# Performance work log

Measured on AMD Instinct MI355X. Metric: run time of the kernel, lower is better.

## Reference

```python
import jax, jax.numpy as jnp
import numpy as np

# static module hyperparameters (match init_kwargs)
DIMS = 1024
HEAD = 16
HD = DIMS // HEAD          # 64
MAX_ITER = 3
MIN_SIZE = 64
MAX_SIZE = 2048
UP_WIN, DOWN_WIN = 1.1, 0.9
UP_DIFF, DOWN_DIFF = 0.05, 0.001
B, T = 2, 1024


def _ln(x, w, eps=1e-5):
    # torch LayerNorm with bias=False (weight only), biased variance
    m = jnp.mean(x, axis=-1, keepdims=True)
    v = jnp.var(x, axis=-1, keepdims=True)
    return (x - m) * jax.lax.rsqrt(v + eps) * w


def setup_inputs() -> dict:
    key = jax.random.key(0)
    ks = jax.random.split(key, 12)

    def lin_w(k, o, i):
        return (jax.random.normal(k, (o, i), dtype=jnp.float32) / np.sqrt(i)).astype(jnp.float32)

    return {
        "x": jax.random.normal(ks[0], (B, T, DIMS), dtype=jnp.float32),
        "Wq": lin_w(ks[1], DIMS, DIMS), "bq": jnp.zeros((DIMS,), jnp.float32),
        "Wk": lin_w(ks[2], DIMS, DIMS),
        "Wv": lin_w(ks[3], DIMS, DIMS), "bv": jnp.zeros((DIMS,), jnp.float32),
        "Wo": lin_w(ks[4], DIMS, DIMS), "bo": jnp.zeros((DIMS,), jnp.float32),
        "lna_w": jnp.ones((DIMS,), jnp.float32),
        "lnb_w": jnp.ones((DIMS,), jnp.float32),
        "lnc_w": jnp.ones((HD,), jnp.float32),
        "lnd_w": jnp.ones((HD,), jnp.float32),
        "lq_w": lin_w(ks[5], HD, HD), "lq_b": jnp.zeros((HD,), jnp.float32),
        "lk_w": lin_w(ks[6], HD, HD), "lk_b": jnp.zeros((HD,), jnp.float32),
        "lv_w": lin_w(ks[7], HD, HD), "lv_b": jnp.zeros((HD,), jnp.float32),
        "threshold": jnp.float32(0.01),
        "temp_base": jnp.float32(1.0),
        "factor": jnp.float32(0.1),
    }


def _focus(x, Wq, bq, Wk, Wv, bv, Wo, bo, lna_w, lnb_w, lnc_w, lnd_w,
           lq_w, lq_b, lk_w, lk_b, lv_w, lv_b, threshold, temp_base, factor):
    b, t, d = x.shape
    q = _ln(x, lna_w) @ Wq.T + bq
    kk = _ln(x, lnb_w) @ Wk.T
    v = _ln(x, lnb_w) @ Wv.T + bv
    sc = HD ** (-0.25)

    def _shape(u):
        return u.reshape(b, t, HEAD, HD).transpose(0, 2, 1, 3)  # [B,H,T,hd]

    q_full = _shape(q * sc)
    k_full = _shape(kk * sc)
    v_full = _shape(v)

    # .item() calls in torch detach these from the graph
    thr = jax.lax.stop_gradient(threshold)
    fac = jax.lax.stop_gradient(factor)
    t0 = jax.lax.stop_gradient(temp_base)

    cw0 = jnp.int32(max(min(t, MAX_SIZE), MIN_SIZE))
    inv_sqrt_e = jnp.float32(1.0 / np.sqrt(HD))  # SDPA default scale
    pos = jnp.arange(t)

    def step(carry, i):
        qcur, prev, attn, cw, temp, done = carry
        # LocalOut projections over full length (out-of-window part masked below)
        qp = qcur @ lq_w.T + lq_b
        kp = k_full @ lk_w.T + lk_b
        vp = v_full @ lv_w.T + lv_b
        sq = _ln(qp, lnc_w)
        sk = _ln(kp, lnd_w)
        tscale = jnp.where(temp > 0, jax.lax.rsqrt(temp), jnp.float32(1.0))
        sq = sq * tscale
        scores = jnp.einsum('bhqd,bhkd->bhqk', sq, sk) * inv_sqrt_e
        in_win = pos < cw
        scores = jnp.where(in_win[None, None, None, :], scores, -jnp.inf)
        probs = jax.nn.softmax(scores, axis=-1)
        out = jnp.einsum('bhqk,bhkd->bhqd', probs, vp)
        # rows >= cur_win stay zero (iter_out buffer semantics)
        iter_out = jnp.where(in_win[None, None, :, None], out, 0.0)

        diff = jnp.mean(jnp.abs(iter_out - prev))
        converged = (diff < thr + fac * diff) & (i > 0)
        upd = (~done) & (~converged)            # continue iterating
        new_done = done | converged

        attn_n = jnp.where(done, attn, iter_out)
        prev_n = jnp.where(upd, iter_out, prev)
        qcur_n = jnp.where(upd, qcur + iter_out, qcur)
        # _next_win
        up = (cw.astype(jnp.float32) * UP_WIN).astype(jnp.int32)
        down = (cw.astype(jnp.float32) * DOWN_WIN).astype(jnp.int32)
        nw = jnp.where(diff > UP_DIFF, up,
                       jnp.where((diff < DOWN_DIFF) & (cw > MIN_SIZE), down, cw))
        nw = jnp.clip(nw, MIN_SIZE, t)
        cw_n = jnp.where(upd, nw, cw)
        temp_n = jnp.where(upd, temp + jnp.float32(0.005), temp)
        return (qcur_n, prev_n, attn_n, cw_n, temp_n, new_done), None

    zeros = jnp.zeros_like(q_full)
    carry0 = (q_full, zeros, zeros, cw0, t0, jnp.array(False))
    (_, _, attn_out, _, _, _), _ = jax.lax.scan(step, carry0, jnp.arange(MAX_ITER))

    output = attn_out.transpose(0, 2, 1, 3).reshape(b, t, d)
    return output @ Wo.T + bo


def reference(x, Wq, bq, Wk, Wv, bv, Wo, bo, lna_w, lnb_w, lnc_w, lnd_w,
              lq_w, lq_b, lk_w, lk_b, lv_w, lv_b, threshold, temp_base, factor):
    return _focus(x, Wq, bq, Wk, Wv, bv, Wo, bo, lna_w, lnb_w, lnc_w, lnd_w,
                  lq_w, lq_b, lk_w, lk_b, lv_w, lv_b, threshold, temp_base, factor)
```

## Files before the change

### kernel.cpp

```cpp
#include <hip/hip_runtime.h>
#include <hip/hip_bf16.h>

#define BDIM 2
#define TDIM 1024
#define DDIM 1024
#define HDIM 16
#define HD   64
#define RROWS (BDIM * TDIM)
#define BH    (BDIM * HDIM)
#define NHE   (BH * TDIM * HD)
#define NHE4  (NHE / 4)
#define DIFF_BLOCKS 512
#define L2E 1.4426950408889634f

typedef __attribute__((ext_vector_type(8))) short short8v;
typedef __attribute__((ext_vector_type(4))) short short4v;
typedef __attribute__((ext_vector_type(8))) _Float16 half8v;
typedef __attribute__((ext_vector_type(4))) _Float16 half4v;
typedef __attribute__((ext_vector_type(4))) float f32x4;

struct FState {
  int   cw;
  float temp;
  int   done;
  int   upd;
  int   done_prev;
  float thr;
  float fac;
  int   pad;
};

static __device__ __forceinline__ unsigned short f2bf(float x) {
  __hip_bfloat16 h = __float2bfloat16(x);
  return __builtin_bit_cast(unsigned short, h);
}
static __device__ __forceinline__ void gload16(const void* g, void* l) {
  __builtin_amdgcn_global_load_lds(
      (const __attribute__((address_space(1))) void*)g,
      (__attribute__((address_space(3))) void*)l, 16, 0, 0);
}

__global__ void init_kernel(FState* st, const float* thr, const float* tb, const float* fac) {
  if (threadIdx.x == 0 && blockIdx.x == 0) {
    st->cw = TDIM;
    st->temp = tb[0];
    st->done = 0;
    st->done_prev = 0;
    st->upd = 1;
    st->thr = thr[0];
    st->fac = fac[0];
  }
}

__global__ __launch_bounds__(256) void ln_x_kernel(
    const float* __restrict__ x, const float* __restrict__ wa, const float* __restrict__ wb,
    _Float16* __restrict__ xaH, _Float16* __restrict__ xbH)
{
  const int row = blockIdx.x;
  const int tid = threadIdx.x;
  const float4 v = reinterpret_cast<const float4*>(x + (size_t)row * DDIM)[tid];
  float s = v.x + v.y + v.z + v.w;
  float q = v.x * v.x + v.y * v.y + v.z * v.z + v.w * v.w;
#pragma unroll
  for (int off = 1; off < 64; off <<= 1) {
    s += __shfl_xor(s, off);
    q += __shfl_xor(q, off);
  }
  __shared__ float ss[4], qq[4];
  const int lane = tid & 63, wv = tid >> 6;
  if (lane == 0) { ss[wv] = s; qq[wv] = q; }
  __syncthreads();
  s = ss[0] + ss[1] + ss[2] + ss[3];
  q = qq[0] + qq[1] + qq[2] + qq[3];
  const float mean = s * (1.0f / DDIM);
  const float var  = q * (1.0f / DDIM) - mean * mean;
  const float inv  = rsqrtf(var + 1e-5f);
  const float4 a4 = reinterpret_cast<const float4*>(wa)[tid];
  const float4 b4 = reinterpret_cast<const float4*>(wb)[tid];
  const float hv[4] = { (v.x - mean) * inv, (v.y - mean) * inv,
                        (v.z - mean) * inv, (v.w - mean) * inv };
  const float av[4] = { a4.x, a4.y, a4.z, a4.w };
  const float bv[4] = { b4.x, b4.y, b4.z, b4.w };
  half4v ha, hb;
#pragma unroll
  for (int j = 0; j < 4; ++j) {
    ha[j] = (_Float16)(hv[j] * av[j]);
    hb[j] = (_Float16)(hv[j] * bv[j]);
  }
  *reinterpret_cast<half4v*>(xaH + (size_t)row * DDIM + tid * 4) = ha;
  *reinterpret_cast<half4v*>(xbH + (size_t)row * DDIM + tid * 4) = hb;
}

__global__ __launch_bounds__(256) void w_cvt_kernel(
    const float* __restrict__ W0, const float* __restrict__ W1,
    const float* __restrict__ W2, const float* __restrict__ W3,
    const float* __restrict__ W4,
    _Float16* __restrict__ O0, _Float16* __restrict__ O1,
    _Float16* __restrict__ O2, _Float16* __restrict__ O3,
    _Float16* __restrict__ O4)
{
  const float* W; _Float16* O;
  switch (blockIdx.y) {
    case 0:  W = W0; O = O0; break;
    case 1:  W = W1; O = O1; break;
    case 2:  W = W2; O = O2; break;
    case 3:  W = W3; O = O3; break;
    default:
      if (blockIdx.x >= 4) return;
      W = W4; O = O4; break;
  }
  const int r = blockIdx.x;
  const int tid = threadIdx.x;
  const float4 v = reinterpret_cast<const float4*>(W + (size_t)r * 1024)[tid];
  half4v h;
  h[0] = (_Float16)v.x; h[1] = (_Float16)v.y;
  h[2] = (_Float16)v.z; h[3] = (_Float16)v.w;
  *reinterpret_cast<half4v*>(O + (size_t)r * 1024 + tid * 4) = h;
}

template<int CMODE>
__global__ __launch_bounds__(256) void gemm_mfma_kernel(
    const _Float16* __restrict__ A0, const _Float16* __restrict__ W0,
    const float* __restrict__ b0, float* __restrict__ C0, float s0,
    const _Float16* __restrict__ A1, const _Float16* __restrict__ W1,
    const float* __restrict__ b1, float* __restrict__ C1, float s1,
    const _Float16* __restrict__ A2, const _Float16* __restrict__ W2,
    const float* __restrict__ b2, float* __restrict__ C2, float s2)
{
  const _Float16* A; const _Float16* W; const float* bias; float* C; float scale;
  switch (blockIdx.z) {
    case 0:  A = A0; W = W0; bias = b0; C = C0; scale = s0; break;
    case 1:  A = A1; W = W1; bias = b1; C = C1; scale = s1; break;
    default: A = A2; W = W2; bias = b2; C = C2; scale = s2; break;
  }
  __shared__ __align__(16) _Float16 As[128 * 32];
  __shared__ __align__(16) _Float16 Ws[128 * 32];
  const int tid = threadIdx.x;
  const int wv = tid >> 6, lane = tid & 63;
  const int wm = wv >> 1, wn = wv & 1;
  const int bm = blockIdx.x;
  const int bn = blockIdx.y;

  const _Float16* gA[2]; const _Float16* gW[2];
  _Float16* lA[2]; _Float16* lW[2];
#pragma unroll
  for (int j = 0; j < 2; ++j) {
    const int chunk = wv * 2 + j;
    const int r = chunk * 16 + (lane >> 2);
    const int ce = (lane & 3) * 8;
    gA[j] = A + (size_t)(bm * 128 + r) * 1024 + ce;
    gW[j] = W + (size_t)(bn * 128 + r) * 1024 + ce;
    lA[j] = As + chunk * 512;
    lW[j] = Ws + chunk * 512;
  }

  f32x4 acc[4][4] = {};
  const int rb = lane & 15;
  const int kb = (lane >> 4) * 8;

  for (int ks = 0; ks < 1024; ks += 32) {
    __syncthreads();
#pragma unroll
    for (int j = 0; j < 2; ++j) {
      gload16(gA[j] + ks, lA[j]);
      gload16(gW[j] + ks, lW[j]);
    }
    __syncthreads();
    half8v af[4], wf[4];
#pragma unroll
    for (int f = 0; f < 4; ++f) {
      af[f] = *reinterpret_cast<const half8v*>(As + (wm * 64 + f * 16 + rb) * 32 + kb);
      wf[f] = *reinterpret_cast<const half8v*>(Ws + (wn * 64 + f * 16 + rb) * 32 + kb);
    }
#pragma unroll
    for (int i = 0; i < 4; ++i)
#pragma unroll
      for (int j2 = 0; j2 < 4; ++j2)
        acc[i][j2] = __builtin_amdgcn_mfma_f32_16x16x32_f16(af[i], wf[j2], acc[i][j2], 0, 0, 0);
  }

#pragma unroll
  for (int j2 = 0; j2 < 4; ++j2) {
    const int n = bn * 128 + wn * 64 + j2 * 16 + (lane & 15);
    const float bv_ = bias ? bias[n] : 0.0f;
#pragma unroll
    for (int i = 0; i < 4; ++i) {
#pragma unroll
      for (int r = 0; r < 4; ++r) {
        const int m = bm * 128 + wm * 64 + i * 16 + (lane >> 4) * 4 + r;
        const float v = (acc[i][j2][r] + bv_) * scale;
        size_t ci;
        if constexpr (CMODE == 0) {
          ci = (size_t)m * 1024 + n;
        } else {
          const int b = m >> 10, t = m & (TDIM - 1);
          ci = ((size_t)(b * HDIM + (n >> 6)) * TDIM + t) * HD + (n & 63);
        }
        C[ci] = v;
      }
    }
  }
}

template<int OUT_MODE, bool DO_LN>
static __device__ __forceinline__ void headproj_body(
    const float* __restrict__ in, unsigned short* __restrict__ out,
    const float* __restrict__ w, const float* __restrict__ bias,
    const float* __restrict__ lnw, float* wl, unsigned short* tT)
{
  const int tid = threadIdx.x;
  for (int idx = tid; idx < 4096; idx += 256) {
    const int d = idx >> 6, i = idx & 63;
    wl[i * 65 + d] = w[idx];
  }
  const int lane = tid & 63, wv = tid >> 6;
  const float bd = bias[lane];
  float lw = 1.0f;
  if constexpr (DO_LN) lw = lnw[lane];
  __syncthreads();
  const int rowBase = blockIdx.x * 32 + wv * 8;
  for (int rr = 0; rr < 8; ++rr) {
    const int row = rowBase + rr;
    const float h = in[(size_t)row * HD + lane];
    float y = bd;
#pragma unroll
    for (int i = 0; i < 64; ++i) {
      const float hv = __uint_as_float((unsigned)__builtin_amdgcn_readlane((int)__float_as_uint(h), i));
      y += wl[i * 65 + lane] * hv;
    }
    if constexpr (DO_LN) {
      float s = y;
#pragma unroll
      for (int off = 1; off < 64; off <<= 1) s += __shfl_xor(s, off);
      const float mean = s * (1.0f / 64.0f);
      const float t0 = y - mean;
      float v2 = t0 * t0;
#pragma unroll
      for (int off = 1; off < 64; off <<= 1) v2 += __shfl_xor(v2, off);
      y = t0 * rsqrtf(v2 * (1.0f / 64.0f) + 1e-5f) * lw;
    }
    if constexpr (OUT_MODE == 0) {
      out[(size_t)row * HD + lane] = f2bf(y);
    } else {
      tT[lane * 34 + wv * 8 + rr] = f2bf(y);
    }
  }
  if constexpr (OUT_MODE == 1) {
    __syncthreads();
    const int hd = tid >> 2, tseg = (tid & 3) * 8;
    const int r0 = blockIdx.x * 32;
    const int bh = r0 >> 10, t0 = r0 & (TDIM - 1);
    short8v v;
#pragma unroll
    for (int i = 0; i < 8; ++i) v[i] = (short)tT[hd * 34 + tseg + i];
    *reinterpret_cast<short8v*>(out + ((size_t)bh * HD + hd) * TDIM + t0 + tseg) = v;
  }
}

__global__ __launch_bounds__(256) void headproj_kv_kernel(
    const float* __restrict__ kin, unsigned short* __restrict__ skb,
    const float* __restrict__ lkw, const float* __restrict__ lkb,
    const float* __restrict__ lnd,
    const float* __restrict__ vin, unsigned short* __restrict__ vpT,
    const float* __restrict__ lvw, const float* __restrict__ lvb)
{
  __shared__ float wl[64 * 65];
  __shared__ unsigned short tT[64 * 34];
  if (blockIdx.y == 0)
    headproj_body<0, true >(kin, skb, lkw, lkb, lnd, wl, tT);
  else
    headproj_body<1, false>(vin, vpT, lvw, lvb, (const float*)nullptr, wl, tT);
}

__global__ __launch_bounds__(256) void attn_mfma_kernel(
    const float* __restrict__ qcur, const unsigned short* __restrict__ sk,
    const unsigned short* __restrict__ vpT, float* __restrict__ io,
    const float* __restrict__ prev, _Float16* __restrict__ attnH,
    const _Float16* __restrict__ lqwH, const float* __restrict__ lqb,
    const float* __restrict__ lnc, float* __restrict__ partials,
    const FState* __restrict__ st, int is_first)
{
  if (st->done) return;
  const int lid = blockIdx.x;
  const int xcd = lid & 7;
  const int rr_ = lid >> 3;
  const int qb  = rr_ & 15;
  const int bh  = (rr_ >> 4) * 8 + xcd;

  const int cw = st->cw;
  const int tid = threadIdx.x;
  const int wv = tid >> 6, lane = tid & 63;
  const int ql = lane & 15, hi = lane >> 4;
  const int qbase = qb * 64 + wv * 16;
  const int q = qbase + ql;
  const size_t baseRow = (size_t)bh * TDIM * HD;
  const size_t baseT   = (size_t)bh * HD * TDIM;
  float* orow = io + baseRow + (size_t)q * HD;
  const float* prow = prev + baseRow + (size_t)q * HD;
  float* qcrow = const_cast<float*>(qcur) + baseRow + (size_t)q * HD;
  const bool wvalid = (qbase < cw);
  _Float16* arow = attnH + (size_t)((bh >> 4) * TDIM + q) * 1024 + (bh & 15) * HD;

  __shared__ __align__(16) unsigned short Kt[2][64 * 64];
  __shared__ __align__(16) unsigned short Vt[2][64 * 64];
  __shared__ __align__(16) unsigned char Plds[4 * 2048];
  __shared__ float wred[4];

  const int sub  = lane >> 3;
  const int colB = (lane & 7) * 16;
  const int scol = (colB ^ (sub << 4)) >> 1;
  const unsigned short* kSrc0 = sk  + baseRow + (size_t)(wv * 16 + sub) * HD + scol;
  const unsigned short* vSrc0 = vpT + baseT  + (size_t)(wv * 16 + sub) * TDIM + scol;

  unsigned char* P = Plds + wv * 2048;
  const unsigned swz = (unsigned)((ql & 7) << 4);
  const unsigned rsw = swz;

#pragma unroll
  for (int jj = 0; jj < 2; ++jj) {
    const int j = wv * 2 + jj;
    gload16(kSrc0 + (size_t)(jj * 8) * HD, &Kt[0][j * 512]);
    gload16(vSrc0 + (size_t)(jj * 8) * TDIM + 0, &Vt[0][j * 512]);
  }

  short8v qf0, qf1;
  if (wvalid) {
    const float tp = st->temp;
    const float ts = (tp > 0.0f ? rsqrtf(tp) : 1.0f) * 0.125f;
    half8v qh0, qh1;
    {
      const f32x4 a0 = *reinterpret_cast<const f32x4*>(qcrow + hi * 8);
      const f32x4 a1 = *reinterpret_cast<const f32x4*>(qcrow + hi * 8 + 4);
      const f32x4 b0 = *reinterpret_cast<const f32x4*>(qcrow + 32 + hi * 8);
      const f32x4 b1 = *reinterpret_cast<const f32x4*>(qcrow + 32 + hi * 8 + 4);
#pragma unroll
      for (int j = 0; j < 4; ++j) {
        qh0[j] = (_Float16)a0[j]; qh0[4 + j] = (_Float16)a1[j];
        qh1[j] = (_Float16)b0[j]; qh1[4 + j] = (_Float16)b1[j];
      }
    }
    f32x4 sp[4];
#pragma unroll
    for (int f = 0; f < 4; ++f) {
      const half8v a0 = *reinterpret_cast<const half8v*>(lqwH + (f * 16 + ql) * 64 + hi * 8);
      const half8v a1 = *reinterpret_cast<const half8v*>(lqwH + (f * 16 + ql) * 64 + 32 + hi * 8);
      f32x4 acc = {};
      acc = __builtin_amdgcn_mfma_f32_16x16x32_f16(a0, qh0, acc, 0, 0, 0);
      acc = __builtin_amdgcn_mfma_f32_16x16x32_f16(a1, qh1, acc, 0, 0, 0);
      sp[f] = acc;
    }
    float sum = 0.f;
#pragma unroll
    for (int f = 0; f < 4; ++f) {
      const f32x4 b4 = *reinterpret_cast<const f32x4*>(lqb + f * 16 + hi * 4);
      sp[f] += b4;
      sum += (sp[f][0] + sp[f][1]) + (sp[f][2] + sp[f][3]);
    }
    sum += __shfl_xor(sum, 16);
    sum += __shfl_xor(sum, 32);
    const float mean = sum * (1.0f / 64.0f);
    float vs = 0.f;
#pragma unroll
    for (int f = 0; f < 4; ++f) {
#pragma unroll
      for (int r = 0; r < 4; ++r) {
        const float t0 = sp[f][r] - mean;
        sp[f][r] = t0;
        vs += t0 * t0;
      }
    }
    vs += __shfl_xor(vs, 16);
    vs += __shfl_xor(vs, 32);
    const float inv = rsqrtf(vs * (1.0f / 64.0f) + 1e-5f);
    const unsigned wb = (unsigned)(ql * 128 + hi * 8);
#pragma unroll
    for (int f = 0; f < 4; ++f) {
      const f32x4 lc = *reinterpret_cast<const f32x4*>(lnc + f * 16 + hi * 4);
      const float y0 = sp[f][0] * inv * lc[0] * ts;
      const float y1 = sp[f][1] * inv * lc[1] * ts;
      const float y2 = sp[f][2] * inv * lc[2] * ts;
      const float y3 = sp[f][3] * inv * lc[3] * ts;
      *reinterpret_cast<unsigned*>(P + ((wb + f * 32)     ^ swz)) =
          (unsigned)f2bf(y0) | ((unsigned)f2bf(y1) << 16);
      *reinterpret_cast<unsigned*>(P + ((wb + f * 32 + 4) ^ swz)) =
          (unsigned)f2bf(y2) | ((unsigned)f2bf(y3) << 16);
    }
    qf0 = *reinterpret_cast<short8v*>(P + ((unsigned)(ql * 128 + hi * 16) ^ swz));
    qf1 = *reinterpret_cast<short8v*>(P + ((unsigned)(ql * 128 + 64 + hi * 16) ^ swz));
  }
  __syncthreads();

  float m = -1e30f, l = 0.f;
  f32x4 o[4] = {};
  const int nch = (cw + 63) >> 6;
  int cur = 0;
  for (int ch = 0; ch < nch; ++ch) {
    const int k0 = ch * 64;
    if (ch + 1 < nch) {
      const int kn = (ch + 1) * 64;
#pragma unroll
      for (int jj = 0; jj < 2; ++jj) {
        const int j = wv * 2 + jj;
        gload16(kSrc0 + (size_t)(kn + jj * 8) * HD, &Kt[cur ^ 1][j * 512]);
        gload16(vSrc0 + (size_t)(jj * 8) * TDIM + kn, &Vt[cur ^ 1][j * 512]);
      }
    }
    if (wvalid) {
      const unsigned char* kt = (const unsigned char*)&Kt[cur][0];
      const unsigned char* vt = (const unsigned char*)&Vt[cur][0];
      f32x4 s[4];
#pragma unroll
      for (int f = 0; f < 4; ++f) {
        const unsigned rb = (unsigned)((f * 16 + ql) * 128);
        const short8v a0 = *reinterpret_cast<const short8v*>(kt + rb + ((unsigned)(hi * 16) ^ rsw));
        const short8v a1 = *reinterpret_cast<const short8v*>(kt + rb + ((unsigned)(64 + hi * 16) ^ rsw));
        f32x4 acc = {};
        acc = __builtin_amdgcn_mfma_f32_16x16x32_bf16(a0, qf0, acc, 0, 0, 0);
        acc = __builtin_amdgcn_mfma_f32_16x16x32_bf16(a1, qf1, acc, 0, 0, 0);
        s[f] = acc;
      }
      float mc = -1e30f;
#pragma unroll
      for (int f = 0; f < 4; ++f) {
#pragma unroll
        for (int r = 0; r < 4; ++r) {
          float v = s[f][r];
          if (k0 + f * 16 + hi * 4 + r >= cw) v = -1e30f;
          s[f][r] = v;
          mc = fmaxf(mc, v);
        }
      }
      mc = fmaxf(mc, __shfl_xor(mc, 16));
      mc = fmaxf(mc, __shfl_xor(mc, 32));
      const float mn = fmaxf(m, mc);
      const float c = __builtin_amdgcn_exp2f((m - mn) * L2E);
      float ls = 0.f;
      unsigned pk[8];
#pragma unroll
      for (int f = 0; f < 4; ++f) {
        const float p0 = __builtin_amdgcn_exp2f((s[f][0] - mn) * L2E);
        const float p1 = __builtin_amdgcn_exp2f((s[f][1] - mn) * L2E);
        const float p2 = __builtin_amdgcn_exp2f((s[f][2] - mn) * L2E);
        const float p3 = __builtin_amdgcn_exp2f((s[f][3] - mn) * L2E);
        ls += (p0 + p1) + (p2 + p3);
        pk[f * 2]     = (unsigned)f2bf(p0) | ((unsigned)f2bf(p1) << 16);
        pk[f * 2 + 1] = (unsigned)f2bf(p2) | ((unsigned)f2bf(p3) << 16);
      }
      ls += __shfl_xor(ls, 16);
      ls += __shfl_xor(ls, 32);
      l = l * c + ls;
      m = mn;
#pragma unroll
      for (int f = 0; f < 4; ++f) o[f] *= c;
      const unsigned wb = (unsigned)(ql * 128 + hi * 8);
#pragma unroll
      for (int f = 0; f < 4; ++f) {
        *reinterpret_cast<unsigned*>(P + ((wb + f * 32)     ^ swz)) = pk[f * 2];
        *reinterpret_cast<unsigned*>(P + ((wb + f * 32 + 4) ^ swz)) = pk[f * 2 + 1];
      }
#pragma unroll
      for (int kh = 0; kh < 2; ++kh) {
        const short8v pb = *reinterpret_cast<short8v*>(
            P + ((unsigned)(ql * 128 + kh * 64 + hi * 16) ^ swz));
#pragma unroll
        for (int f = 0; f < 4; ++f) {
          const unsigned rb = (unsigned)((f * 16 + ql) * 128);
          const short8v av = *reinterpret_cast<const short8v*>(
              vt + rb + ((unsigned)(kh * 64 + hi * 16) ^ rsw));
          o[f] = __builtin_amdgcn_mfma_f32_16x16x32_bf16(av, pb, o[f], 0, 0, 0);
        }
      }
    }
    __syncthreads();
    cur ^= 1;
  }

  float pd = 0.0f;
  if (wvalid) {
    const bool valid = (q < cw);
    const float invl = valid ? (1.0f / l) : 0.0f;
#pragma unroll
    for (int f = 0; f < 4; ++f) {
      const f32x4 vo = o[f] * invl;
      *reinterpret_cast<f32x4*>(orow + f * 16 + hi * 4) = vo;
      half4v h4;
      h4[0] = (_Float16)vo[0]; h4[1] = (_Float16)vo[1];
      h4[2] = (_Float16)vo[2]; h4[3] = (_Float16)vo[3];
      *reinterpret_cast<half4v*>(arow + f * 16 + hi * 4) = h4;
      const f32x4 qv = *reinterpret_cast<const f32x4*>(qcrow + f * 16 + hi * 4);
      *reinterpret_cast<f32x4*>(qcrow + f * 16 + hi * 4) = qv + vo;
      if (!is_first) {
        const f32x4 pv = *reinterpret_cast<const f32x4*>(prow + f * 16 + hi * 4);
        pd += fabsf(vo[0] - pv[0]) + fabsf(vo[1] - pv[1]) +
              fabsf(vo[2] - pv[2]) + fabsf(vo[3] - pv[3]);
      } else {
        pd += fabsf(vo[0]) + fabsf(vo[1]) + fabsf(vo[2]) + fabsf(vo[3]);
      }
    }
  } else {
    const f32x4 z = {0.f, 0.f, 0.f, 0.f};
    const half4v hz = { (_Float16)0.f, (_Float16)0.f, (_Float16)0.f, (_Float16)0.f };
#pragma unroll
    for (int f = 0; f < 4; ++f) {
      *reinterpret_cast<f32x4*>(orow + f * 16 + hi * 4) = z;
      *reinterpret_cast<half4v*>(arow + f * 16 + hi * 4) = hz;
      if (!is_first) {
        const f32x4 pv = *reinterpret_cast<const f32x4*>(prow + f * 16 + hi * 4);
        pd += fabsf(pv[0]) + fabsf(pv[1]) + fabsf(pv[2]) + fabsf(pv[3]);
      }
    }
  }

#pragma unroll
  for (int off = 1; off < 64; off <<= 1) pd += __shfl_xor(pd, off);
  if (lane == 0) wred[wv] = pd;
  __syncthreads();
  if (tid == 0)
    partials[lid] = wred[0] + wred[1] + wred[2] + wred[3];
}

__global__ __launch_bounds__(256) void state_update_kernel(
    FState* __restrict__ st, const float* __restrict__ partials, int iter)
{
  const int tid = threadIdx.x;
  float s = 0.0f;
  for (int i = tid; i < DIFF_BLOCKS; i += 256) s += partials[i];
  __shared__ float red[256];
  red[tid] = s;
  __syncthreads();
  for (int off = 128; off > 0; off >>= 1) {
    if (tid < off) red[tid] += red[tid + off];
    __syncthreads();
  }
  if (tid == 0) {
    const int done_prev = st->done;
    st->done_prev = done_prev;
    if (!done_prev) {
      const float diff = red[0] * (1.0f / (float)NHE);
      const bool conv = (diff < st->thr + st->fac * diff) && (iter > 0);
      st->upd  = conv ? 0 : 1;
      st->done = conv ? 1 : 0;
      if (!conv) {
        const int cw = st->cw;
        const int up = (int)((float)cw * 1.1f);
        const int dn = (int)((float)cw * 0.9f);
        int nw = (diff > 0.05f) ? up : ((diff < 0.001f && cw > 64) ? dn : cw);
        nw = nw < 64 ? 64 : (nw > TDIM ? TDIM : nw);
        st->cw = nw;
        st->temp += 0.005f;
      }
    } else {
      st->upd = 0;
    }
  }
}

extern "C" void kernel_launch(void* const* d_in, const int* in_sizes, int n_in,
                              void* d_out, int out_size, void* d_ws, size_t ws_size,
                              hipStream_t stream)
{
  const float* x   = (const float*)d_in[0];
  const float* Wq  = (const float*)d_in[1];
  const float* bq  = (const float*)d_in[2];
  const float* Wk  = (const float*)d_in[3];
  const float* Wv  = (const float*)d_in[4];
  const float* bv  = (const float*)d_in[5];
  const float* Wo  = (const float*)d_in[6];
  const float* bo  = (const float*)d_in[7];
  const float* lna = (const float*)d_in[8];
  const float* lnb = (const float*)d_in[9];
  const float* lnc = (const float*)d_in[10];
  const float* lnd = (const float*)d_in[11];
  const float* lqw = (const float*)d_in[12];
  const float* lqb = (const float*)d_in[13];
  const float* lkw = (const float*)d_in[14];
  const float* lkb = (const float*)d_in[15];
  const float* lvw = (const float*)d_in[16];
  const float* lvb = (const float*)d_in[17];
  const float* thr = (const float*)d_in[18];
  const float* tb  = (const float*)d_in[19];
  const float* fac = (const float*)d_in[20];
  float* out = (float*)d_out;

  float* f0   = (float*)d_ws;
  float* qcur = f0;
  float* io0  = f0 + (size_t)NHE;
  float* io1  = f0 + 2 * (size_t)NHE;
  _Float16* h0   = (_Float16*)(f0 + 3 * (size_t)NHE);
  _Float16* xaH  = h0;
  _Float16* attnH = h0;
  _Float16* xbH  = h0 + (size_t)RROWS * 1024;
  _Float16* WqH  = xbH + (size_t)RROWS * 1024;
  _Float16* WkH  = WqH + (size_t)1048576;
  _Float16* WvH  = WkH + (size_t)1048576;
  _Float16* WoH  = WvH + (size_t)1048576;
  _Float16* lqwH = WoH + (size_t)1048576;
  unsigned short* skb = (unsigned short*)(lqwH + 4096);
  unsigned short* vpT = skb + (size_t)NHE;
  float* partials = (float*)(vpT + (size_t)NHE);
  FState* st = (FState*)(partials + DIFF_BLOCKS);

  constexpr float SC = 0.35355339059327379f;

  hipLaunchKernelGGL(init_kernel, dim3(1), dim3(64), 0, stream, st, thr, tb, fac);
  hipLaunchKernelGGL(ln_x_kernel, dim3(RROWS), dim3(256), 0, stream, x, lna, lnb, xaH, xbH);
  hipLaunchKernelGGL(w_cvt_kernel, dim3(1024, 5), dim3(256), 0, stream,
                     Wq, Wk, Wv, Wo, lqw, WqH, WkH, WvH, WoH, lqwH);

  hipLaunchKernelGGL((gemm_mfma_kernel<1>), dim3(16, 8, 3), dim3(256), 0, stream,
                     xaH, WqH, bq, qcur, SC,
                     xbH, WkH, (const float*)nullptr, io0, SC,
                     xbH, WvH, bv, io1, 1.0f);

  hipLaunchKernelGGL(headproj_kv_kernel, dim3(1024, 2), dim3(256), 0, stream,
                     io0, skb, lkw, lkb, lnd, io1, vpT, lvw, lvb);

  for (int it = 0; it < 3; ++it) {
    float* io   = (it & 1) ? io1 : io0;
    float* prev = (it & 1) ? io0 : io1;
    hipLaunchKernelGGL(attn_mfma_kernel, dim3(DIFF_BLOCKS), dim3(256), 0, stream,
                       qcur, skb, vpT, io, prev, attnH, lqwH, lqb, lnc,
                       partials, st, it == 0 ? 1 : 0);
    hipLaunchKernelGGL(state_update_kernel, dim3(1), dim3(256), 0, stream,
                       st, partials, it);
  }

  hipLaunchKernelGGL((gemm_mfma_kernel<0>), dim3(16, 8, 1), dim3(256), 0, stream,
                     attnH, WoH, bo, out, 1.0f,
                     attnH, WoH, bo, out, 1.0f,
                     attnH, WoH, bo, out, 1.0f);
}
```

Before: 171.6 us.

## Split attention key range across two wave groups with flash-decoding style merge

Doubles the attention block to 512 threads. Two groups of four waves each handle half of the key window (first 512 keys and the rest) in 32-key chunks, and their partial softmax state (m, l, o) is merged through LDS at the end. It also adds a lazy rescale that only updates the running max when it grows by more than a threshold, and skips the masking pass on full chunks. The aim is more parallelism and shorter serial loops per wave. The cost is higher register and LDS pressure, an extra merge step, and idle second-half waves when the window is at most 512.

```diff
diff --git a/kernel.cpp b/kernel.cpp
--- a/kernel.cpp
+++ b/kernel.cpp
@@ -272,7 +272,7 @@
     headproj_body<1, false>(vin, vpT, lvw, lvb, (const float*)nullptr, wl, tT);
 }
 
-__global__ __launch_bounds__(256) void attn_mfma_kernel(
+__global__ __launch_bounds__(512) void attn_mfma_kernel(
     const float* __restrict__ qcur, const unsigned short* __restrict__ sk,
     const unsigned short* __restrict__ vpT, float* __restrict__ io,
     const float* __restrict__ prev, _Float16* __restrict__ attnH,
@@ -290,8 +290,9 @@
   const int cw = st->cw;
   const int tid = threadIdx.x;
   const int wv = tid >> 6, lane = tid & 63;
+  const int wq = wv & 3, wk = wv >> 2;
   const int ql = lane & 15, hi = lane >> 4;
-  const int qbase = qb * 64 + wv * 16;
+  const int qbase = qb * 64 + wq * 16;
   const int q = qbase + ql;
   const size_t baseRow = (size_t)bh * TDIM * HD;
   const size_t baseT   = (size_t)bh * HD * TDIM;
@@ -301,26 +302,32 @@
   const bool wvalid = (qbase < cw);
   _Float16* arow = attnH + (size_t)((bh >> 4) * TDIM + q) * 1024 + (bh & 15) * HD;
 
-  __shared__ __align__(16) unsigned short Kt[2][64 * 64];
-  __shared__ __align__(16) unsigned short Vt[2][64 * 64];
-  __shared__ __align__(16) unsigned char Plds[4 * 2048];
-  __shared__ float wred[4];
+  __shared__ __align__(16) unsigned char KV[2][2][2][4096];
+  __shared__ __align__(16) unsigned char PJ[8][2048];
+  __shared__ float wred[8];
 
   const int sub  = lane >> 3;
   const int colB = (lane & 7) * 16;
-  const int scol = (colB ^ (sub << 4)) >> 1;
-  const unsigned short* kSrc0 = sk  + baseRow + (size_t)(wv * 16 + sub) * HD + scol;
-  const unsigned short* vSrc0 = vpT + baseT  + (size_t)(wv * 16 + sub) * TDIM + scol;
-
-  unsigned char* P = Plds + wv * 2048;
-  const unsigned swz = (unsigned)((ql & 7) << 4);
-  const unsigned rsw = swz;
-
-#pragma unroll
-  for (int jj = 0; jj < 2; ++jj) {
-    const int j = wv * 2 + jj;
-    gload16(kSrc0 + (size_t)(jj * 8) * HD, &Kt[0][j * 512]);
-    gload16(vSrc0 + (size_t)(jj * 8) * TDIM + 0, &Vt[0][j * 512]);
+  const int scolK = (colB ^ (sub << 4)) >> 1;
+  const int vrow  = lane >> 2;
+  const int vcolB = (lane & 3) * 16;
+  const int scolV = (vcolB ^ ((vrow & 3) << 4)) >> 1;
+
+  const int kb0 = wk * 512;
+  const unsigned short* kSrc0 = sk  + baseRow + (size_t)(kb0 + wq * 8 + sub) * HD + scolK;
+  const unsigned short* vSrc0 = vpT + baseT  + (size_t)(wq * 16 + vrow) * TDIM + scolV;
+
+  unsigned char* pj = (unsigned char*)PJ[wv];
+  const unsigned swz8 = (unsigned)((ql & 7) << 4);
+  const unsigned swzP = (unsigned)((ql & 3) << 4);
+
+  const int nch0 = (min(cw, 512) + 31) >> 5;
+  const int nch1 = (cw > 512) ? ((cw - 512 + 31) >> 5) : 0;
+  const int nchOwn = wk ? nch1 : nch0;
+
+  if (nchOwn > 0) {
+    gload16(kSrc0, &KV[wk][0][0][wq * 1024]);
+    gload16(vSrc0 + kb0, &KV[wk][0][1][wq * 1024]);
   }
 
   short8v qf0, qf1;
@@ -380,133 +387,152 @@
       const float y1 = sp[f][1] * inv * lc[1] * ts;
       const float y2 = sp[f][2] * inv * lc[2] * ts;
       const float y3 = sp[f][3] * inv * lc[3] * ts;
-      *reinterpret_cast<unsigned*>(P + ((wb + f * 32)     ^ swz)) =
+      *reinterpret_cast<unsigned*>(pj + ((wb + f * 32)     ^ swz8)) =
           (unsigned)f2bf(y0) | ((unsigned)f2bf(y1) << 16);
-      *reinterpret_cast<unsigned*>(P + ((wb + f * 32 + 4) ^ swz)) =
+      *reinterpret_cast<unsigned*>(pj + ((wb + f * 32 + 4) ^ swz8)) =
           (unsigned)f2bf(y2) | ((unsigned)f2bf(y3) << 16);
     }
-    qf0 = *reinterpret_cast<short8v*>(P + ((unsigned)(ql * 128 + hi * 16) ^ swz));
-    qf1 = *reinterpret_cast<short8v*>(P + ((unsigned)(ql * 128 + 64 + hi * 16) ^ swz));
+    qf0 = *reinterpret_cast<short8v*>(pj + ((unsigned)(ql * 128 + hi * 16) ^ swz8));
+    qf1 = *reinterpret_cast<short8v*>(pj + ((unsigned)(ql * 128 + 64 + hi * 16) ^ swz8));
   }
   __syncthreads();
 
   float m = -1e30f, l = 0.f;
   f32x4 o[4] = {};
-  const int nch = (cw + 63) >> 6;
   int cur = 0;
-  for (int ch = 0; ch < nch; ++ch) {
-    const int k0 = ch * 64;
-    if (ch + 1 < nch) {
-      const int kn = (ch + 1) * 64;
-#pragma unroll
-      for (int jj = 0; jj < 2; ++jj) {
-        const int j = wv * 2 + jj;
-        gload16(kSrc0 + (size_t)(kn + jj * 8) * HD, &Kt[cur ^ 1][j * 512]);
-        gload16(vSrc0 + (size_t)(jj * 8) * TDIM + kn, &Vt[cur ^ 1][j * 512]);
-      }
-    }
-    if (wvalid) {
-      const unsigned char* kt = (const unsigned char*)&Kt[cur][0];
-      const unsigned char* vt = (const unsigned char*)&Vt[cur][0];
-      f32x4 s[4];
-#pragma unroll
-      for (int f = 0; f < 4; ++f) {
+  for (int ch = 0; ch < nch0; ++ch) {
+    if (ch + 1 < nchOwn) {
+      gload16(kSrc0 + (size_t)((ch + 1) * 32) * HD, &KV[wk][cur ^ 1][0][wq * 1024]);
+      gload16(vSrc0 + kb0 + (ch + 1) * 32, &KV[wk][cur ^ 1][1][wq * 1024]);
+    }
+    if (wvalid && ch < nchOwn) {
+      const int k0 = kb0 + ch * 32;
+      const unsigned char* kt = &KV[wk][cur][0][0];
+      const unsigned char* vt = &KV[wk][cur][1][0];
+      f32x4 s[2];
+#pragma unroll
+      for (int f = 0; f < 2; ++f) {
         const unsigned rb = (unsigned)((f * 16 + ql) * 128);
-        const short8v a0 = *reinterpret_cast<const short8v*>(kt + rb + ((unsigned)(hi * 16) ^ rsw));
-        const short8v a1 = *reinterpret_cast<const short8v*>(kt + rb + ((unsigned)(64 + hi * 16) ^ rsw));
+        const short8v a0 = *reinterpret_cast<const short8v*>(kt + rb + ((unsigned)(hi * 16) ^ swz8));
+        const short8v a1 = *reinterpret_cast<const short8v*>(kt + rb + ((unsigned)(64 + hi * 16) ^ swz8));
         f32x4 acc = {};
         acc = __builtin_amdgcn_mfma_f32_16x16x32_bf16(a0, qf0, acc, 0, 0, 0);
         acc = __builtin_amdgcn_mfma_f32_16x16x32_bf16(a1, qf1, acc, 0, 0, 0);
         s[f] = acc;
       }
       float mc = -1e30f;
-#pragma unroll
-      for (int f = 0; f < 4; ++f) {
-#pragma unroll
-        for (int r = 0; r < 4; ++r) {
-          float v = s[f][r];
-          if (k0 + f * 16 + hi * 4 + r >= cw) v = -1e30f;
-          s[f][r] = v;
-          mc = fmaxf(mc, v);
-        }
+      if (k0 + 32 > cw) {
+#pragma unroll
+        for (int f = 0; f < 2; ++f)
+#pragma unroll
+          for (int r = 0; r < 4; ++r) {
+            float v = s[f][r];
+            if (k0 + f * 16 + hi * 4 + r >= cw) v = -1e30f;
+            s[f][r] = v;
+            mc = fmaxf(mc, v);
+          }
+      } else {
+#pragma unroll
+        for (int f = 0; f < 2; ++f)
+#pragma unroll
+          for (int r = 0; r < 4; ++r) mc = fmaxf(mc, s[f][r]);
       }
       mc = fmaxf(mc, __shfl_xor(mc, 16));
       mc = fmaxf(mc, __shfl_xor(mc, 32));
-      const float mn = fmaxf(m, mc);
-      const float c = __builtin_amdgcn_exp2f((m - mn) * L2E);
+      if (__any(mc > m + 8.0f)) {
+        const float mn = fmaxf(m, mc);
+        const float c = __builtin_amdgcn_exp2f((m - mn) * L2E);
+        l *= c;
+#pragma unroll
+        for (int f = 0; f < 4; ++f) o[f] *= c;
+        m = mn;
+      }
       float ls = 0.f;
-      unsigned pk[8];
-#pragma unroll
-      for (int f = 0; f < 4; ++f) {
-        const float p0 = __builtin_amdgcn_exp2f((s[f][0] - mn) * L2E);
-        const float p1 = __builtin_amdgcn_exp2f((s[f][1] - mn) * L2E);
-        const float p2 = __builtin_amdgcn_exp2f((s[f][2] - mn) * L2E);
-        const float p3 = __builtin_amdgcn_exp2f((s[f][3] - mn) * L2E);
+      unsigned pk[4];
+#pragma unroll
+      for (int f = 0; f < 2; ++f) {
+        const float p0 = __builtin_amdgcn_exp2f((s[f][0] - m) * L2E);
+        const float p1 = __builtin_amdgcn_exp2f((s[f][1] - m) * L2E);
+        const float p2 = __builtin_amdgcn_exp2f((s[f][2] - m) * L2E);
+        const float p3 = __builtin_amdgcn_exp2f((s[f][3] - m) * L2E);
         ls += (p0 + p1) + (p2 + p3);
         pk[f * 2]     = (unsigned)f2bf(p0) | ((unsigned)f2bf(p1) << 16);
         pk[f * 2 + 1] = (unsigned)f2bf(p2) | ((unsigned)f2bf(p3) << 16);
       }
       ls += __shfl_xor(ls, 16);
       ls += __shfl_xor(ls, 32);
-      l = l * c + ls;
-      m = mn;
-#pragma unroll
-      for (int f = 0; f < 4; ++f) o[f] *= c;
-      const unsigned wb = (unsigned)(ql * 128 + hi * 8);
+      l += ls;
+      const unsigned pbase = (unsigned)(ql * 64);
+#pragma unroll
+      for (int f = 0; f < 2; ++f) {
+        *reinterpret_cast<unsigned*>(pj + pbase + (((unsigned)(f * 32 + hi * 8))     ^ swzP)) = pk[f * 2];
+        *reinterpret_cast<unsigned*>(pj + pbase + (((unsigned)(f * 32 + hi * 8 + 4)) ^ swzP)) = pk[f * 2 + 1];
+      }
+      const short8v pb = *reinterpret_cast<short8v*>(pj + pbase + ((unsigned)(hi * 16) ^ swzP));
 #pragma unroll
       for (int f = 0; f < 4; ++f) {
-        *reinterpret_cast<unsigned*>(P + ((wb + f * 32)     ^ swz)) = pk[f * 2];
-        *reinterpret_cast<unsigned*>(P + ((wb + f * 32 + 4) ^ swz)) = pk[f * 2 + 1];
-      }
-#pragma unroll
-      for (int kh = 0; kh < 2; ++kh) {
-        const short8v pb = *reinterpret_cast<short8v*>(
-            P + ((unsigned)(ql * 128 + kh * 64 + hi * 16) ^ swz));
-#pragma unroll
-        for (int f = 0; f < 4; ++f) {
-          const unsigned rb = (unsigned)((f * 16 + ql) * 128);
-          const short8v av = *reinterpret_cast<const short8v*>(
-              vt + rb + ((unsigned)(kh * 64 + hi * 16) ^ rsw));
-          o[f] = __builtin_amdgcn_mfma_f32_16x16x32_bf16(av, pb, o[f], 0, 0, 0);
-        }
+        const unsigned vb = (unsigned)((f * 16 + ql) * 64) + ((unsigned)(hi * 16) ^ swzP);
+        const short8v av = *reinterpret_cast<const short8v*>(vt + vb);
+        o[f] = __builtin_amdgcn_mfma_f32_16x16x32_bf16(av, pb, o[f], 0, 0, 0);
       }
     }
     __syncthreads();
     cur ^= 1;
   }
 
+  float* Obuf = reinterpret_cast<float*>(&KV[0][0][0][0]);
+  if (wk == 1 && wvalid) {
+    if (hi == 0) {
+      Obuf[4352 + wq * 16 + ql] = m;
+      Obuf[4416 + wq * 16 + ql] = l;
+    }
+#pragma unroll
+    for (int f = 0; f < 4; ++f)
+      *reinterpret_cast<f32x4*>(&Obuf[(wq * 16 + ql) * 68 + f * 16 + hi * 4]) = o[f];
+  }
+  __syncthreads();
+
   float pd = 0.0f;
-  if (wvalid) {
-    const bool valid = (q < cw);
-    const float invl = valid ? (1.0f / l) : 0.0f;
-#pragma unroll
-    for (int f = 0; f < 4; ++f) {
-      const f32x4 vo = o[f] * invl;
-      *reinterpret_cast<f32x4*>(orow + f * 16 + hi * 4) = vo;
-      half4v h4;
-      h4[0] = (_Float16)vo[0]; h4[1] = (_Float16)vo[1];
-      h4[2] = (_Float16)vo[2]; h4[3] = (_Float16)vo[3];
-      *reinterpret_cast<half4v*>(arow + f * 16 + hi * 4) = h4;
-      const f32x4 qv = *reinterpret_cast<const f32x4*>(qcrow + f * 16 + hi * 4);
-      *reinterpret_cast<f32x4*>(qcrow + f * 16 + hi * 4) = qv + vo;
-      if (!is_first) {
-        const f32x4 pv = *reinterpret_cast<const f32x4*>(prow + f * 16 + hi * 4);
-        pd += fabsf(vo[0] - pv[0]) + fabsf(vo[1] - pv[1]) +
-              fabsf(vo[2] - pv[2]) + fabsf(vo[3] - pv[3]);
-      } else {
-        pd += fabsf(vo[0]) + fabsf(vo[1]) + fabsf(vo[2]) + fabsf(vo[3]);
-      }
-    }
-  } else {
-    const f32x4 z = {0.f, 0.f, 0.f, 0.f};
-    const half4v hz = { (_Float16)0.f, (_Float16)0.f, (_Float16)0.f, (_Float16)0.f };
-#pragma unroll
-    for (int f = 0; f < 4; ++f) {
-      *reinterpret_cast<f32x4*>(orow + f * 16 + hi * 4) = z;
-      *reinterpret_cast<half4v*>(arow + f * 16 + hi * 4) = hz;
-      if (!is_first) {
-        const f32x4 pv = *reinterpret_cast<const f32x4*>(prow + f * 16 + hi * 4);
-        pd += fabsf(pv[0]) + fabsf(pv[1]) + fabsf(pv[2]) + fabsf(pv[3]);
+  if (wk == 0) {
+    if (wvalid) {
+      const float m1 = Obuf[4352 + wq * 16 + ql];
+      const float l1 = Obuf[4416 + wq * 16 + ql];
+      const float mn = fmaxf(m, m1);
+      const float c0 = __builtin_amdgcn_exp2f((m - mn) * L2E);
+      const float c1 = __builtin_amdgcn_exp2f((m1 - mn) * L2E);
+      const float lt = l * c0 + l1 * c1;
+      const bool valid = (q < cw);
+      const float invl = valid ? (1.0f / lt) : 0.0f;
+#pragma unroll
+      for (int f = 0; f < 4; ++f) {
+        const f32x4 o1 = *reinterpret_cast<const f32x4*>(&Obuf[(wq * 16 + ql) * 68 + f * 16 + hi * 4]);
+        const f32x4 vo = (o[f] * c0 + o1 * c1) * invl;
+        *reinterpret_cast<f32x4*>(orow + f * 16 + hi * 4) = vo;
+        half4v h4;
+        h4[0] = (_Float16)vo[0]; h4[1] = (_Float16)vo[1];
+        h4[2] = (_Float16)vo[2]; h4[3] = (_Float16)vo[3];
+        *reinterpret_cast<half4v*>(arow + f * 16 + hi * 4) = h4;
+        const f32x4 qv = *reinterpret_cast<const f32x4*>(qcrow + f * 16 + hi * 4);
+        *reinterpret_cast<f32x4*>(qcrow + f * 16 + hi * 4) = qv + vo;
+        if (!is_first) {
+          const f32x4 pv = *reinterpret_cast<const f32x4*>(prow + f * 16 + hi * 4);
+          pd += fabsf(vo[0] - pv[0]) + fabsf(vo[1] - pv[1]) +
+                fabsf(vo[2] - pv[2]) + fabsf(vo[3] - pv[3]);
+        } else {
+          pd += fabsf(vo[0]) + fabsf(vo[1]) + fabsf(vo[2]) + fabsf(vo[3]);
+        }
+      }
+    } else {
+      const f32x4 z = {0.f, 0.f, 0.f, 0.f};
+      const half4v hz = { (_Float16)0.f, (_Float16)0.f, (_Float16)0.f, (_Float16)0.f };
+#pragma unroll
+      for (int f = 0; f < 4; ++f) {
+        *reinterpret_cast<f32x4*>(orow + f * 16 + hi * 4) = z;
+        *reinterpret_cast<half4v*>(arow + f * 16 + hi * 4) = hz;
+        if (!is_first) {
+          const f32x4 pv = *reinterpret_cast<const f32x4*>(prow + f * 16 + hi * 4);
+          pd += fabsf(pv[0]) + fabsf(pv[1]) + fabsf(pv[2]) + fabsf(pv[3]);
+        }
       }
     }
   }
@@ -516,7 +542,8 @@
   if (lane == 0) wred[wv] = pd;
   __syncthreads();
   if (tid == 0)
-    partials[lid] = wred[0] + wred[1] + wred[2] + wred[3];
+    partials[lid] = wred[0] + wred[1] + wred[2] + wred[3] +
+                    wred[4] + wred[5] + wred[6] + wred[7];
 }
 
 __global__ __launch_bounds__(256) void state_update_kernel(
@@ -618,7 +645,7 @@
   for (int it = 0; it < 3; ++it) {
     float* io   = (it & 1) ? io1 : io0;
     float* prev = (it & 1) ? io0 : io1;
-    hipLaunchKernelGGL(attn_mfma_kernel, dim3(DIFF_BLOCKS), dim3(256), 0, stream,
+    hipLaunchKernelGGL(attn_mfma_kernel, dim3(DIFF_BLOCKS), dim3(512), 0, stream,
                        qcur, skb, vpT, io, prev, attnH, lqwH, lqb, lnc,
                        partials, st, it == 0 ? 1 : 0);
     hipLaunchKernelGGL(state_update_kernel, dim3(1), dim3(256), 0, stream,
```

Result: no change. 171.3 us (-0.2%).
